# Optimization experiments

Hardware: AMD Instinct MI355X
Metric: run time of the kernel (lower is better)

The kernel has to match this reference:

```python
import jax, jax.numpy as jnp
import numpy as np

N, E, D, H, C = 100000, 1600000, 128, 256, 40


def setup_inputs() -> dict:
    key = jax.random.key(0)
    ks = jax.random.split(key, 10)
    x = jax.random.normal(ks[0], (N, D), dtype=jnp.float32)
    src = jax.random.randint(ks[1], (E,), 0, N, dtype=jnp.int32)
    dst = jax.random.randint(ks[2], (E,), 0, N, dtype=jnp.int32)
    # GIN layer 1 MLP (bias-free), kaiming-uniform-like scale 1/sqrt(fan_in)
    w1a = jax.random.normal(ks[3], (D, H), dtype=jnp.float32) / np.sqrt(D)
    w1b = jax.random.normal(ks[4], (H, H), dtype=jnp.float32) / np.sqrt(H)
    # GIN layer 2 MLP
    w2a = jax.random.normal(ks[5], (H, H), dtype=jnp.float32) / np.sqrt(H)
    w2b = jax.random.normal(ks[6], (H, H), dtype=jnp.float32) / np.sqrt(H)
    # eps initialized to 0 per reset_parameters
    eps1 = jnp.zeros((), dtype=jnp.float32)
    eps2 = jnp.zeros((), dtype=jnp.float32)
    # final classifier fc (with bias)
    fc_w = jax.random.normal(ks[7], (H, C), dtype=jnp.float32) / np.sqrt(H)
    fc_b = jax.random.normal(ks[8], (C,), dtype=jnp.float32) * 0.01
    return {"x": x, "src": src, "dst": dst,
            "eps1": eps1, "w1a": w1a, "w1b": w1b,
            "eps2": eps2, "w2a": w2a, "w2b": w2b,
            "fc_w": fc_w, "fc_b": fc_b}


def reference(x, src, dst, eps1, w1a, w1b, eps2, w2a, w2b, fc_w, fc_b):
    n = x.shape[0]

    def gin_layer(h, eps, wa, wb):
        # GINConv sum-aggregation: scatter-add neighbor feats over edges
        agg = jax.ops.segment_sum(h[src], dst, num_segments=n)  # [N, d]
        rst = (1.0 + eps) * h + agg
        # 2-layer bias-free MLP with ReLU between
        return jax.nn.relu(rst @ wa) @ wb

    h = jax.nn.relu(gin_layer(x, eps1, w1a, w1b))   # layer + outer activation
    h = jax.nn.relu(gin_layer(h, eps2, w2a, w2b))   # dropout p=0 -> identity
    return h @ fc_w + fc_b                           # [N, C]
```

## Files before the change

### kernel.cpp

```cpp
#include <hip/hip_runtime.h>

#define N_NODES 100000
#define N_EDGES 1600000
#define DIM_IN  128
#define DIM_H   256
#define DIM_C   40

#define NB   391
#define NBLK 391
#define CHUNK 4096
#define ECAP 6144

#define CVT_BLOCKS 25000
#define WCVT_BLOCKS 1280

typedef unsigned short bf16_t;
typedef __attribute__((ext_vector_type(8))) short short8;
typedef __attribute__((ext_vector_type(4))) float f32x4;

__device__ __forceinline__ bf16_t f2b(float f) {
    unsigned int u = __float_as_uint(f);
    unsigned int r = (u + 0x7fffu + ((u >> 16) & 1u)) >> 16;
    return (bf16_t)r;
}

__device__ __forceinline__ void gl_lds16(const void* gsrc, void* ldst) {
    __builtin_amdgcn_global_load_lds(
        (const __attribute__((address_space(1))) void*)gsrc,
        (__attribute__((address_space(3))) void*)ldst,
        16, 0, 0);
}


__global__ __launch_bounds__(256) void k_prep(
    const int* __restrict__ dst, int* __restrict__ cnt2,
    const float* __restrict__ x, signed char* __restrict__ x8, float* __restrict__ xs,
    const float* __restrict__ w1a, const float* __restrict__ w1b,
    const float* __restrict__ w2a, const float* __restrict__ w2b,
    const float* __restrict__ fcw,
    bf16_t* __restrict__ o1a, bf16_t* __restrict__ o1b,
    bf16_t* __restrict__ o2a, bf16_t* __restrict__ o2b, bf16_t* __restrict__ ofc,
    int* __restrict__ ticket)
{
    __shared__ int h[NB];
    int blk = blockIdx.x, t = threadIdx.x;

    if (blk < NBLK) {
        if (blk == 0 && t == 0) *ticket = 0;
        for (int i = t; i < NB; i += 256) h[i] = 0;
        __syncthreads();
        int base = blk * CHUNK;
        int end = min(base + CHUNK, N_EDGES);
        for (int i = base + t; i < end; i += 256)
            atomicAdd(&h[dst[i] >> 8], 1);
        __syncthreads();
        for (int i = t; i < NB; i += 256) cnt2[blk * NB + i] = h[i];
        return;
    }
    blk -= NBLK;

    if (blk < CVT_BLOCKS) {
        int gid = blk * 256 + t;
        int u = gid >> 6, lane = gid & 63;
        float2 v = *(const float2*)(x + (size_t)u * 128 + lane * 2);
        float m = fmaxf(fabsf(v.x), fabsf(v.y));
        #pragma unroll
        for (int d = 1; d < 64; d <<= 1)
            m = fmaxf(m, __shfl_xor(m, d, 64));
        float inv = (m > 0.f) ? 127.f / m : 0.f;
        int q0 = (int)rintf(v.x * inv);
        int q1 = (int)rintf(v.y * inv);
        unsigned short pk = (unsigned short)((q0 & 0xff) | ((q1 & 0xff) << 8));
        *(unsigned short*)(x8 + ((unsigned)u << 7) + lane * 2) = pk;
        if (lane == 0) xs[u] = (m > 0.f) ? m * (1.f / 127.f) : 0.f;
        return;
    }
    blk -= CVT_BLOCKS;

    int r = blk >> 8;
    int idx = (blk & 255) * 256 + t;
    const float* in; bf16_t* out; int K, N, Npad;
    switch (r) {
        case 0: in = w1a; out = o1a; K = 128; N = 256; Npad = 256; break;
        case 1: in = w1b; out = o1b; K = 256; N = 256; Npad = 256; break;
        case 2: in = w2a; out = o2a; K = 256; N = 256; Npad = 256; break;
        case 3: in = w2b; out = o2b; K = 256; N = 256; Npad = 256; break;
        default: in = fcw; out = ofc; K = 256; N = 40;  Npad = 128; break;
    }
    if (idx >= Npad * K) return;
    int n = idx / K, k = idx - n * K;
    float v = (n < N) ? in[(size_t)k * N + n] : 0.f;
    out[idx] = f2b(v);
}


__global__ void k_bscanA(const int* __restrict__ cnt2, int* __restrict__ basep,
                         int* __restrict__ btot, int* __restrict__ ticket,
                         int* __restrict__ boff) {
    __shared__ int s[512];
    __shared__ int isLast;
    int t = threadIdx.x, b = blockIdx.x;
    int v = (t < NBLK) ? cnt2[t * NB + b] : 0;
    s[t] = v;
    __syncthreads();
    #pragma unroll
    for (int d = 1; d < 512; d <<= 1) {
        int tv = (t >= d) ? s[t - d] : 0;
        __syncthreads();
        s[t] += tv;
        __syncthreads();
    }
    if (t < NBLK) basep[t * NB + b] = s[t] - v;
    if (t == 511) atomicExch(&btot[b], s[511]);
    __syncthreads();
    if (t == 0) {
        __threadfence();
        int old = atomicAdd(ticket, 1);
        isLast = (old == NB - 1);
    }
    __syncthreads();
    if (!isLast) return;

    __threadfence();
    int v2 = (t < NB) ? atomicAdd(&btot[t], 0) : 0;
    s[t] = v2;
    __syncthreads();
    #pragma unroll
    for (int d = 1; d < 512; d <<= 1) {
        int tv = (t >= d) ? s[t - d] : 0;
        __syncthreads();
        s[t] += tv;
        __syncthreads();
    }
    if (t < NB) boff[t] = s[t] - v2;
    if (t == NB - 1) boff[NB] = s[t];
}

__global__ void k_bscatter(const int* __restrict__ src, const int* __restrict__ dst,
                           const int* __restrict__ basep, const int* __restrict__ boff,
                           int* __restrict__ ebuf, int e) {
    __shared__ int cur[NB];
    int t = threadIdx.x, blk = blockIdx.x;
    for (int i = t; i < NB; i += 256) cur[i] = basep[blk * NB + i] + boff[i];
    __syncthreads();
    int base = blk * CHUNK;
    int end = min(base + CHUNK, e);
    for (int i = base + t; i < end; i += 256) {
        int sv = src[i], dv = dst[i];
        int pos = atomicAdd(&cur[dv >> 8], 1);
        ebuf[pos] = sv | ((dv & 255) << 24);
    }
}

__global__ __launch_bounds__(256) void k_build(const int* __restrict__ ebuf,
                                               const int* __restrict__ boff,
                                               int* __restrict__ off,
                                               int* __restrict__ csr) {
    __shared__ int ec[ECAP];
    __shared__ int h[256];
    __shared__ int cur[256];
    int t = threadIdx.x, b = blockIdx.x;
    int node0 = b << 8;
    int e0 = boff[b], e1 = boff[b + 1];
    int ne = e1 - e0;
    bool fits = (ne <= ECAP);
    h[t] = 0;
    __syncthreads();
    if (fits) {
        for (int i = t; i < ne; i += 256) {
            int p = ebuf[e0 + i];
            ec[i] = p;
            atomicAdd(&h[(unsigned)p >> 24], 1);
        }
    } else {
        for (int i = t; i < ne; i += 256)
            atomicAdd(&h[(unsigned)ebuf[e0 + i] >> 24], 1);
    }
    __syncthreads();
    int mydeg = h[t];
    #pragma unroll
    for (int d = 1; d < 256; d <<= 1) {
        int tv = (t >= d) ? h[t - d] : 0;
        __syncthreads();
        h[t] += tv;
        __syncthreads();
    }
    int node = node0 + t;
    if (node < N_NODES) off[node + 1] = e0 + h[t];
    if (b == 0 && t == 0) off[0] = 0;
    cur[t] = e0 + h[t] - mydeg;
    __syncthreads();
    if (fits) {
        for (int i = t; i < ne; i += 256) {
            int p = ec[i];
            int pos = atomicAdd(&cur[(unsigned)p >> 24], 1);
            csr[pos] = p & 0xFFFFFF;
        }
    } else {
        for (int i = t; i < ne; i += 256) {
            int p = ebuf[e0 + i];
            int pos = atomicAdd(&cur[(unsigned)p >> 24], 1);
            csr[pos] = p & 0xFFFFFF;
        }
    }
}


__global__ void k_agg_i8(const signed char* __restrict__ h8, const float* __restrict__ hs,
                         const int* __restrict__ off, const int* __restrict__ csr,
                         const float* __restrict__ eps_p,
                         bf16_t* __restrict__ rst, int n) {
    int gid = blockIdx.x * blockDim.x + threadIdx.x;
    int u = __builtin_amdgcn_readfirstlane(gid >> 6);
    int lane = threadIdx.x & 63;
    if (u >= n) return;

    float acc0 = 0.f, acc1 = 0.f;
    int r0 = off[u], r1 = off[u + 1];
    unsigned loff = lane * 2u;

    for (int base = r0; base < r1; base += 64) {
        int m = r1 - base; if (m > 64) m = 64;
        int li = (lane < m) ? lane : (m - 1);
        int iv = csr[base + li];
        for (int c = 0; c < m; c += 16) {
            int s[16]; float sc[16]; unsigned v[16];
            #pragma unroll
            for (int t = 0; t < 16; t++)
                s[t] = __builtin_amdgcn_readlane(iv, c + t);
            #pragma unroll
            for (int t = 0; t < 16; t++)
                sc[t] = (c + t < m) ? hs[s[t]] : 0.f;
            #pragma unroll
            for (int t = 0; t < 16; t++)
                v[t] = *(const unsigned short*)(h8 + (((unsigned)s[t] << 7) + loff));
            #pragma unroll
            for (int t = 0; t < 16; t++) {
                acc0 += (float)(int)(signed char)(v[t] & 0xffu) * sc[t];
                acc1 += (float)(int)(signed char)(v[t] >> 8) * sc[t];
            }
        }
    }

    float scu = hs[u] * (1.0f + eps_p[0]);
    unsigned vu = *(const unsigned short*)(h8 + (((unsigned)u << 7) + loff));
    float o0 = (float)(int)(signed char)(vu & 0xffu) * scu + acc0;
    float o1 = (float)(int)(signed char)(vu >> 8) * scu + acc1;
    *(unsigned int*)(rst + ((unsigned)u << 7) + lane * 2) =
        (unsigned int)f2b(o0) | ((unsigned int)f2b(o1) << 16);
}


__global__ void k_agg_u8(const unsigned char* __restrict__ h8,
                         const float* __restrict__ hs,
                         const int* __restrict__ off, const int* __restrict__ csr,
                         const float* __restrict__ eps_p,
                         bf16_t* __restrict__ rst, int n) {
    int gid = blockIdx.x * blockDim.x + threadIdx.x;
    int u = __builtin_amdgcn_readfirstlane(gid >> 6);
    int lane = threadIdx.x & 63;
    if (u >= n) return;

    float acc[4] = {0.f, 0.f, 0.f, 0.f};
    int r0 = off[u], r1 = off[u + 1];
    unsigned loff = lane * 4u;

    for (int base = r0; base < r1; base += 64) {
        int m = r1 - base; if (m > 64) m = 64;
        int li = (lane < m) ? lane : (m - 1);
        int iv = csr[base + li];
        for (int c = 0; c < m; c += 16) {
            int s[16]; float sc[16]; unsigned int v[16];
            #pragma unroll
            for (int t = 0; t < 16; t++)
                s[t] = __builtin_amdgcn_readlane(iv, c + t);
            #pragma unroll
            for (int t = 0; t < 16; t++)
                sc[t] = (c + t < m) ? hs[s[t]] : 0.f;
            #pragma unroll
            for (int t = 0; t < 16; t++)
                v[t] = *(const unsigned int*)(h8 + (((unsigned)s[t] << 8) + loff));
            #pragma unroll
            for (int t = 0; t < 16; t++) {
                acc[0] += (float)(v[t] & 0xffu) * sc[t];
                acc[1] += (float)((v[t] >> 8) & 0xffu) * sc[t];
                acc[2] += (float)((v[t] >> 16) & 0xffu) * sc[t];
                acc[3] += (float)(v[t] >> 24) * sc[t];
            }
        }
    }

    float ep = 1.0f + eps_p[0];
    unsigned int vu = *(const unsigned int*)(h8 + (((unsigned)u << 8) + loff));
    float scu = hs[u] * ep;
    float o0 = (float)(vu & 0xffu) * scu + acc[0];
    float o1 = (float)((vu >> 8) & 0xffu) * scu + acc[1];
    float o2 = (float)((vu >> 16) & 0xffu) * scu + acc[2];
    float o3 = (float)(vu >> 24) * scu + acc[3];
    uint2 ov;
    ov.x = (unsigned int)f2b(o0) | ((unsigned int)f2b(o1) << 16);
    ov.y = (unsigned int)f2b(o2) | ((unsigned int)f2b(o3) << 16);
    *(uint2*)(rst + (size_t)u * 256 + lane * 4) = ov;
}


#define TS_STRIDE 264

template <int K1, bool OUT8, bool FUSE_FC>
__global__ __launch_bounds__(512, 4) void k_mlp(
    const bf16_t* __restrict__ A, const bf16_t* __restrict__ W1t,
    const bf16_t* __restrict__ W2t, bf16_t* __restrict__ H,
    unsigned char* __restrict__ H8, float* __restrict__ Hs,
    const bf16_t* __restrict__ FCt, const float* __restrict__ fc_b,
    float* __restrict__ Cout, int M)
{
    __shared__ __align__(16) bf16_t As[2][64 * 32];
    __shared__ __align__(16) bf16_t Bs[2][256 * 32];
    __shared__ __align__(16) bf16_t Ts[64 * TS_STRIDE];
    __shared__ int rmax[64];

    int tid = threadIdx.x;
    int wave = tid >> 6, lane = tid & 63;
    int l15 = lane & 15, quad = lane >> 4;
    int bm = blockIdx.x * 64;
    int wn = wave * 32;

    auto stage1 = [&](int k0, int b) {
        if (tid < 256) {
            int row = tid >> 2, k8 = (tid & 3) * 8;
            int gr = bm + row; if (gr >= M) gr = M - 1;
            gl_lds16(A + (size_t)gr * K1 + k0 + k8, &As[b][tid * 8]);
        }
        {
            int c = tid;
            int row = c >> 2, k8 = (c & 3) * 8;
            gl_lds16(W1t + (size_t)row * K1 + k0 + k8, &Bs[b][c * 8]);
        }
        {
            int c = tid + 512;
            int row = c >> 2, k8 = (c & 3) * 8;
            gl_lds16(W1t + (size_t)row * K1 + k0 + k8, &Bs[b][c * 8]);
        }
    };
    auto stage2 = [&](int k0, int b) {
        {
            int c = tid;
            int row = c >> 2, k8 = (c & 3) * 8;
            gl_lds16(W2t + (size_t)row * 256 + k0 + k8, &Bs[b][c * 8]);
        }
        {
            int c = tid + 512;
            int row = c >> 2, k8 = (c & 3) * 8;
            gl_lds16(W2t + (size_t)row * 256 + k0 + k8, &Bs[b][c * 8]);
        }
    };

    f32x4 acc[4][2];
    #pragma unroll
    for (int i = 0; i < 4; i++)
        #pragma unroll
        for (int j = 0; j < 2; j++) acc[i][j] = 0.f;

    constexpr int NS1 = K1 / 32;
    stage1(0, 0);
    for (int k = 0; k < NS1; k++) {
        int cur = k & 1;
        if (k + 1 < NS1) {
            stage1((k + 1) * 32, cur ^ 1);
            if (tid < 256) { asm volatile("s_waitcnt vmcnt(3)" ::: "memory"); }
            else           { asm volatile("s_waitcnt vmcnt(2)" ::: "memory"); }
        } else {
            asm volatile("s_waitcnt vmcnt(0)" ::: "memory");
        }
        __builtin_amdgcn_sched_barrier(0);
        __builtin_amdgcn_s_barrier();

        short8 af[4], bfv[2];
        #pragma unroll
        for (int i = 0; i < 4; i++)
            af[i] = *(const short8*)&As[cur][(i * 16 + l15) * 32 + quad * 8];
        #pragma unroll
        for (int j = 0; j < 2; j++)
            bfv[j] = *(const short8*)&Bs[cur][(wn + j * 16 + l15) * 32 + quad * 8];

        #pragma unroll
        for (int i = 0; i < 4; i++)
            #pragma unroll
            for (int j = 0; j < 2; j++)
                acc[i][j] = __builtin_amdgcn_mfma_f32_16x16x32_bf16(af[i], bfv[j], acc[i][j], 0, 0, 0);

        asm volatile("s_waitcnt lgkmcnt(0)" ::: "memory");
        __builtin_amdgcn_sched_barrier(0);
        __builtin_amdgcn_s_barrier();
    }

    #pragma unroll
    for (int i = 0; i < 4; i++)
        #pragma unroll
        for (int j = 0; j < 2; j++) {
            int row = i * 16 + quad * 4;
            int col = wn + j * 16 + l15;
            #pragma unroll
            for (int r = 0; r < 4; r++)
                Ts[(row + r) * TS_STRIDE + col] = f2b(fmaxf(acc[i][j][r], 0.f));
        }

    #pragma unroll
    for (int i = 0; i < 4; i++)
        #pragma unroll
        for (int j = 0; j < 2; j++) acc[i][j] = 0.f;
    __syncthreads();

    stage2(0, 0);
    for (int k = 0; k < 8; k++) {
        int cur = k & 1;
        if (k + 1 < 8) {
            stage2((k + 1) * 32, cur ^ 1);
            asm volatile("s_waitcnt vmcnt(2)" ::: "memory");
        } else {
            asm volatile("s_waitcnt vmcnt(0)" ::: "memory");
        }
        __builtin_amdgcn_sched_barrier(0);
        __builtin_amdgcn_s_barrier();

        short8 af[4], bfv[2];
        #pragma unroll
        for (int i = 0; i < 4; i++)
            af[i] = *(const short8*)&Ts[(i * 16 + l15) * TS_STRIDE + k * 32 + quad * 8];
        #pragma unroll
        for (int j = 0; j < 2; j++)
            bfv[j] = *(const short8*)&Bs[cur][(wn + j * 16 + l15) * 32 + quad * 8];

        #pragma unroll
        for (int i = 0; i < 4; i++)
            #pragma unroll
            for (int j = 0; j < 2; j++)
                acc[i][j] = __builtin_amdgcn_mfma_f32_16x16x32_bf16(af[i], bfv[j], acc[i][j], 0, 0, 0);

        asm volatile("s_waitcnt lgkmcnt(0)" ::: "memory");
        __builtin_amdgcn_sched_barrier(0);
        __builtin_amdgcn_s_barrier();
    }

    if constexpr (OUT8) {
        if (tid < 64) rmax[tid] = 0;
        __syncthreads();
        #pragma unroll
        for (int i = 0; i < 4; i++)
            #pragma unroll
            for (int r = 0; r < 4; r++) {
                float m = 0.f;
                #pragma unroll
                for (int j = 0; j < 2; j++) m = fmaxf(m, acc[i][j][r]);
                atomicMax(&rmax[i * 16 + quad * 4 + r], __float_as_int(m));
            }
        __syncthreads();
        #pragma unroll
        for (int i = 0; i < 4; i++) {
            #pragma unroll
            for (int r = 0; r < 4; r++) {
                int row = i * 16 + quad * 4 + r;
                int rowg = bm + row;
                if (rowg >= M) continue;
                float rm = __int_as_float(rmax[row]);
                float inv = (rm > 0.f) ? 255.f / rm : 0.f;
                #pragma unroll
                for (int j = 0; j < 2; j++) {
                    int col = wn + j * 16 + l15;
                    float v = fmaxf(acc[i][j][r], 0.f);
                    unsigned q = (unsigned)(v * inv + 0.5f);
                    if (q > 255u) q = 255u;
                    H8[(size_t)rowg * 256 + col] = (unsigned char)q;
                }
                if (wave == 0 && l15 == 0)
                    Hs[rowg] = rm * (1.f / 255.f);
            }
        }
    } else if constexpr (FUSE_FC) {
        #pragma unroll
        for (int i = 0; i < 4; i++)
            #pragma unroll
            for (int j = 0; j < 2; j++) {
                int row = i * 16 + quad * 4;
                int col = wn + j * 16 + l15;
                #pragma unroll
                for (int r = 0; r < 4; r++)
                    Ts[(row + r) * TS_STRIDE + col] = f2b(fmaxf(acc[i][j][r], 0.f));
            }
        __syncthreads();

        f32x4 acc3[3];
        #pragma unroll
        for (int j = 0; j < 3; j++) acc3[j] = 0.f;

        auto stage3 = [&](int k0, int b) {
            if (tid < 256) {
                int row = tid >> 2, k8 = (tid & 3) * 8;
                gl_lds16(FCt + (size_t)row * 256 + k0 + k8, &Bs[b][tid * 8]);
            }
        };

        stage3(0, 0);
        for (int k = 0; k < 8; k++) {
            int cur = k & 1;
            if (k + 1 < 8) {
                stage3((k + 1) * 32, cur ^ 1);
                if (tid < 256) { asm volatile("s_waitcnt vmcnt(1)" ::: "memory"); }
            } else {
                if (tid < 256) { asm volatile("s_waitcnt vmcnt(0)" ::: "memory"); }
            }
            __builtin_amdgcn_sched_barrier(0);
            __builtin_amdgcn_s_barrier();

            if (tid < 256) {
                short8 af = *(const short8*)&Ts[(wave * 16 + l15) * TS_STRIDE + k * 32 + quad * 8];
                #pragma unroll
                for (int j = 0; j < 3; j++) {
                    short8 bfv = *(const short8*)&Bs[cur][(j * 16 + l15) * 32 + quad * 8];
                    acc3[j] = __builtin_amdgcn_mfma_f32_16x16x32_bf16(af, bfv, acc3[j], 0, 0, 0);
                }
                asm volatile("s_waitcnt lgkmcnt(0)" ::: "memory");
            }
            __builtin_amdgcn_sched_barrier(0);
            __builtin_amdgcn_s_barrier();
        }

        if (tid < 256) {
            #pragma unroll
            for (int j = 0; j < 3; j++) {
                int col = j * 16 + l15;
                if (col >= DIM_C) continue;
                float bv = fc_b[col];
                #pragma unroll
                for (int r = 0; r < 4; r++) {
                    int rowg = bm + wave * 16 + quad * 4 + r;
                    if (rowg < M)
                        Cout[(size_t)rowg * DIM_C + col] = acc3[j][r] + bv;
                }
            }
        }
    } else {
        #pragma unroll
        for (int j = 0; j < 2; j++) {
            int col = wn + j * 16 + l15;
            #pragma unroll
            for (int i = 0; i < 4; i++) {
                #pragma unroll
                for (int r = 0; r < 4; r++) {
                    int rowg = bm + i * 16 + quad * 4 + r;
                    if (rowg < M)
                        H[(size_t)rowg * 256 + col] = f2b(fmaxf(acc[i][j][r], 0.f));
                }
            }
        }
    }
}


static inline size_t rnd256(size_t x) { return (x + 255) & ~(size_t)255; }

extern "C" void kernel_launch(void* const* d_in, const int* in_sizes, int n_in,
                              void* d_out, int out_size, void* d_ws, size_t ws_size,
                              hipStream_t stream) {
    const float* x    = (const float*)d_in[0];
    const int*   src  = (const int*)d_in[1];
    const int*   dst  = (const int*)d_in[2];
    const float* eps1 = (const float*)d_in[3];
    const float* w1a  = (const float*)d_in[4];
    const float* w1b  = (const float*)d_in[5];
    const float* eps2 = (const float*)d_in[6];
    const float* w2a  = (const float*)d_in[7];
    const float* w2b  = (const float*)d_in[8];
    const float* fc_w = (const float*)d_in[9];
    const float* fc_b = (const float*)d_in[10];
    float* out = (float*)d_out;

    char* w = (char*)d_ws;
    int* off  = (int*)w; w += rnd256(sizeof(int) * (size_t)(N_NODES + 1));
    int* csr  = (int*)w; w += rnd256(sizeof(int) * (size_t)N_EDGES);
    int* cnt2  = (int*)w; w += rnd256(sizeof(int) * (size_t)NBLK * NB);
    int* basep = (int*)w; w += rnd256(sizeof(int) * (size_t)NBLK * NB);
    int* btot  = (int*)w; w += rnd256(sizeof(int) * 512);
    int* boff  = (int*)w; w += rnd256(sizeof(int) * (NB + 1));
    bf16_t* w1a_t = (bf16_t*)w; w += rnd256(2 * (size_t)DIM_H * DIM_IN);
    bf16_t* w1b_t = (bf16_t*)w; w += rnd256(2 * (size_t)DIM_H * DIM_H);
    bf16_t* w2a_t = (bf16_t*)w; w += rnd256(2 * (size_t)DIM_H * DIM_H);
    bf16_t* w2b_t = (bf16_t*)w; w += rnd256(2 * (size_t)DIM_H * DIM_H);
    bf16_t* fc_t  = (bf16_t*)w; w += rnd256(2 * (size_t)128 * DIM_H);
    signed char* x8 = (signed char*)w; w += rnd256((size_t)N_NODES * DIM_IN);
    float* xs = (float*)w; w += rnd256(sizeof(float) * (size_t)N_NODES);
    unsigned char* h8 = (unsigned char*)w; w += rnd256((size_t)N_NODES * DIM_H);
    float* hs = (float*)w; w += rnd256(sizeof(float) * (size_t)N_NODES);
    bf16_t* R12 = (bf16_t*)w; w += rnd256(2 * (size_t)N_NODES * DIM_H);
    bf16_t* R3  = (bf16_t*)w; w += rnd256(2 * (size_t)N_NODES * DIM_H);

    bf16_t* rst1 = R12;
    int* ebuf = (int*)R3;
    int* ticket = btot + 500;

    k_prep<<<NBLK + CVT_BLOCKS + WCVT_BLOCKS, 256, 0, stream>>>(
        dst, cnt2, x, x8, xs, w1a, w1b, w2a, w2b, fc_w,
        w1a_t, w1b_t, w2a_t, w2b_t, fc_t, ticket);

    k_bscanA<<<NB, 512, 0, stream>>>(cnt2, basep, btot, ticket, boff);
    k_bscatter<<<NBLK, 256, 0, stream>>>(src, dst, basep, boff, ebuf, N_EDGES);
    k_build<<<NB, 256, 0, stream>>>(ebuf, boff, off, csr);

    const int agg_blocks = (N_NODES * 64 + 255) / 256;
    const int mlp_blocks = (N_NODES + 63) / 64;

    k_agg_i8<<<agg_blocks, 256, 0, stream>>>(x8, xs, off, csr, eps1, rst1, N_NODES);
    k_mlp<DIM_IN, true, false><<<mlp_blocks, 512, 0, stream>>>(
        rst1, w1a_t, w1b_t, nullptr, h8, hs, nullptr, nullptr, nullptr, N_NODES);

    k_agg_u8<<<agg_blocks, 256, 0, stream>>>(h8, hs, off, csr, eps2, (bf16_t*)R3, N_NODES);
    k_mlp<DIM_H, false, true><<<mlp_blocks, 512, 0, stream>>>(
        (bf16_t*)R3, w2a_t, w2b_t, nullptr, nullptr, nullptr, fc_t, fc_b, out, N_NODES);
}
```

Before: 421.4 us.

## Pre-swizzle weights into MFMA fragment layout and load A directly into registers

```diff
diff --git a/kernel.cpp b/kernel.cpp
--- a/kernel.cpp
+++ b/kernel.cpp
@@ -85,12 +85,15 @@
         case 1: in = w1b; out = o1b; K = 256; N = 256; Npad = 256; break;
         case 2: in = w2a; out = o2a; K = 256; N = 256; Npad = 256; break;
         case 3: in = w2b; out = o2b; K = 256; N = 256; Npad = 256; break;
-        default: in = fcw; out = ofc; K = 256; N = 40;  Npad = 128; break;
+        default: in = fcw; out = ofc; K = 256; N = 40;  Npad = 64;  break;
     }
     if (idx >= Npad * K) return;
     int n = idx / K, k = idx - n * K;
     float v = (n < N) ? in[(size_t)k * N + n] : 0.f;
-    out[idx] = f2b(v);
+    int kstep = k >> 5, quad = (k >> 3) & 3, e = k & 7;
+    int tt = n >> 4, l15 = n & 15;
+    size_t opos = (size_t)kstep * (Npad * 32) + ((tt * 4 + quad) * 16 + l15) * 8 + e;
+    out[opos] = f2b(v);
 }
 
 
@@ -307,14 +310,13 @@
 #define TS_STRIDE 264
 
 template <int K1, bool OUT8, bool FUSE_FC>
-__global__ __launch_bounds__(512, 4) void k_mlp(
+__global__ __launch_bounds__(256, 2) void k_mlp(
     const bf16_t* __restrict__ A, const bf16_t* __restrict__ W1t,
     const bf16_t* __restrict__ W2t, bf16_t* __restrict__ H,
     unsigned char* __restrict__ H8, float* __restrict__ Hs,
     const bf16_t* __restrict__ FCt, const float* __restrict__ fc_b,
     float* __restrict__ Cout, int M)
 {
-    __shared__ __align__(16) bf16_t As[2][64 * 32];
     __shared__ __align__(16) bf16_t Bs[2][256 * 32];
     __shared__ __align__(16) bf16_t Ts[64 * TS_STRIDE];
     __shared__ int rmax[64];
@@ -323,81 +325,65 @@
     int wave = tid >> 6, lane = tid & 63;
     int l15 = lane & 15, quad = lane >> 4;
     int bm = blockIdx.x * 64;
-    int wn = wave * 32;
-
-    auto stage1 = [&](int k0, int b) {
-        if (tid < 256) {
-            int row = tid >> 2, k8 = (tid & 3) * 8;
-            int gr = bm + row; if (gr >= M) gr = M - 1;
-            gl_lds16(A + (size_t)gr * K1 + k0 + k8, &As[b][tid * 8]);
-        }
-        {
-            int c = tid;
-            int row = c >> 2, k8 = (c & 3) * 8;
-            gl_lds16(W1t + (size_t)row * K1 + k0 + k8, &Bs[b][c * 8]);
-        }
-        {
-            int c = tid + 512;
-            int row = c >> 2, k8 = (c & 3) * 8;
-            gl_lds16(W1t + (size_t)row * K1 + k0 + k8, &Bs[b][c * 8]);
+
+    auto stageB = [&](const bf16_t* W, int kstep, int b) {
+        #pragma unroll
+        for (int l = 0; l < 4; l++) {
+            int c = l * 256 + tid;
+            gl_lds16(W + ((size_t)kstep * 1024 + c) * 8, &Bs[b][c * 8]);
         }
     };
-    auto stage2 = [&](int k0, int b) {
-        {
-            int c = tid;
-            int row = c >> 2, k8 = (c & 3) * 8;
-            gl_lds16(W2t + (size_t)row * 256 + k0 + k8, &Bs[b][c * 8]);
-        }
-        {
-            int c = tid + 512;
-            int row = c >> 2, k8 = (c & 3) * 8;
-            gl_lds16(W2t + (size_t)row * 256 + k0 + k8, &Bs[b][c * 8]);
-        }
-    };
-
-    f32x4 acc[4][2];
+
+    f32x4 acc[4][4];
     #pragma unroll
     for (int i = 0; i < 4; i++)
         #pragma unroll
-        for (int j = 0; j < 2; j++) acc[i][j] = 0.f;
+        for (int j = 0; j < 4; j++) acc[i][j] = 0.f;
 
     constexpr int NS1 = K1 / 32;
-    stage1(0, 0);
+    short8 afr[NS1][4];
+    #pragma unroll
+    for (int ks = 0; ks < NS1; ks++)
+        #pragma unroll
+        for (int i = 0; i < 4; i++) {
+            int gr = bm + i * 16 + l15; if (gr >= M) gr = M - 1;
+            afr[ks][i] = *(const short8*)(A + (size_t)gr * K1 + ks * 32 + quad * 8);
+        }
+
+    stageB(W1t, 0, 0);
+    #pragma unroll
     for (int k = 0; k < NS1; k++) {
         int cur = k & 1;
         if (k + 1 < NS1) {
-            stage1((k + 1) * 32, cur ^ 1);
-            if (tid < 256) { asm volatile("s_waitcnt vmcnt(3)" ::: "memory"); }
-            else           { asm volatile("s_waitcnt vmcnt(2)" ::: "memory"); }
+            stageB(W1t, k + 1, cur ^ 1);
+            asm volatile("s_waitcnt vmcnt(4)" ::: "memory");
         } else {
             asm volatile("s_waitcnt vmcnt(0)" ::: "memory");
         }
         __builtin_amdgcn_sched_barrier(0);
         __builtin_amdgcn_s_barrier();
 
-        short8 af[4], bfv[2];
+        short8 bfv[4];
+        #pragma unroll
+        for (int j = 0; j < 4; j++)
+            bfv[j] = *(const short8*)&Bs[cur][((wave * 4 + j) * 64 + lane) * 8];
+
         #pragma unroll
         for (int i = 0; i < 4; i++)
-            af[i] = *(const short8*)&As[cur][(i * 16 + l15) * 32 + quad * 8];
-        #pragma unroll
-        for (int j = 0; j < 2; j++)
-            bfv[j] = *(const short8*)&Bs[cur][(wn + j * 16 + l15) * 32 + quad * 8];
-
-        #pragma unroll
-        for (int i = 0; i < 4; i++)
-            #pragma unroll
-            for (int j = 0; j < 2; j++)
-                acc[i][j] = __builtin_amdgcn_mfma_f32_16x16x32_bf16(af[i], bfv[j], acc[i][j], 0, 0, 0);
+            #pragma unroll
+            for (int j = 0; j < 4; j++)
+                acc[i][j] = __builtin_amdgcn_mfma_f32_16x16x32_bf16(afr[k][i], bfv[j], acc[i][j], 0, 0, 0);
 
         asm volatile("s_waitcnt lgkmcnt(0)" ::: "memory");
         __builtin_amdgcn_sched_barrier(0);
         __builtin_amdgcn_s_barrier();
     }
 
+    int wn = wave * 64;
     #pragma unroll
     for (int i = 0; i < 4; i++)
         #pragma unroll
-        for (int j = 0; j < 2; j++) {
+        for (int j = 0; j < 4; j++) {
             int row = i * 16 + quad * 4;
             int col = wn + j * 16 + l15;
             #pragma unroll
@@ -408,33 +394,34 @@
     #pragma unroll
     for (int i = 0; i < 4; i++)
         #pragma unroll
-        for (int j = 0; j < 2; j++) acc[i][j] = 0.f;
-    __syncthreads();
-
-    stage2(0, 0);
+        for (int j = 0; j < 4; j++) acc[i][j] = 0.f;
+    __syncthreads();
+
+    stageB(W2t, 0, 0);
+    #pragma unroll
     for (int k = 0; k < 8; k++) {
         int cur = k & 1;
         if (k + 1 < 8) {
-            stage2((k + 1) * 32, cur ^ 1);
-            asm volatile("s_waitcnt vmcnt(2)" ::: "memory");
+            stageB(W2t, k + 1, cur ^ 1);
+            asm volatile("s_waitcnt vmcnt(4)" ::: "memory");
         } else {
             asm volatile("s_waitcnt vmcnt(0)" ::: "memory");
         }
         __builtin_amdgcn_sched_barrier(0);
         __builtin_amdgcn_s_barrier();
 
-        short8 af[4], bfv[2];
+        short8 af[4], bfv[4];
         #pragma unroll
         for (int i = 0; i < 4; i++)
             af[i] = *(const short8*)&Ts[(i * 16 + l15) * TS_STRIDE + k * 32 + quad * 8];
         #pragma unroll
-        for (int j = 0; j < 2; j++)
-            bfv[j] = *(const short8*)&Bs[cur][(wn + j * 16 + l15) * 32 + quad * 8];
+        for (int j = 0; j < 4; j++)
+            bfv[j] = *(const short8*)&Bs[cur][((wave * 4 + j) * 64 + lane) * 8];
 
         #pragma unroll
         for (int i = 0; i < 4; i++)
             #pragma unroll
-            for (int j = 0; j < 2; j++)
+            for (int j = 0; j < 4; j++)
                 acc[i][j] = __builtin_amdgcn_mfma_f32_16x16x32_bf16(af[i], bfv[j], acc[i][j], 0, 0, 0);
 
         asm volatile("s_waitcnt lgkmcnt(0)" ::: "memory");
@@ -451,7 +438,7 @@
             for (int r = 0; r < 4; r++) {
                 float m = 0.f;
                 #pragma unroll
-                for (int j = 0; j < 2; j++) m = fmaxf(m, acc[i][j][r]);
+                for (int j = 0; j < 4; j++) m = fmaxf(m, acc[i][j][r]);
                 atomicMax(&rmax[i * 16 + quad * 4 + r], __float_as_int(m));
             }
         __syncthreads();
@@ -465,7 +452,7 @@
                 float rm = __int_as_float(rmax[row]);
                 float inv = (rm > 0.f) ? 255.f / rm : 0.f;
                 #pragma unroll
-                for (int j = 0; j < 2; j++) {
+                for (int j = 0; j < 4; j++) {
                     int col = wn + j * 16 + l15;
                     float v = fmaxf(acc[i][j][r], 0.f);
                     unsigned q = (unsigned)(v * inv + 0.5f);
@@ -480,7 +467,7 @@
         #pragma unroll
         for (int i = 0; i < 4; i++)
             #pragma unroll
-            for (int j = 0; j < 2; j++) {
+            for (int j = 0; j < 4; j++) {
                 int row = i * 16 + quad * 4;
                 int col = wn + j * 16 + l15;
                 #pragma unroll
@@ -493,55 +480,50 @@
         #pragma unroll
         for (int j = 0; j < 3; j++) acc3[j] = 0.f;
 
-        auto stage3 = [&](int k0, int b) {
-            if (tid < 256) {
-                int row = tid >> 2, k8 = (tid & 3) * 8;
-                gl_lds16(FCt + (size_t)row * 256 + k0 + k8, &Bs[b][tid * 8]);
-            }
+        auto stage3 = [&](int kstep, int b) {
+            gl_lds16(FCt + ((size_t)kstep * 256 + tid) * 8, &Bs[b][tid * 8]);
         };
 
         stage3(0, 0);
+        #pragma unroll
         for (int k = 0; k < 8; k++) {
             int cur = k & 1;
             if (k + 1 < 8) {
-                stage3((k + 1) * 32, cur ^ 1);
-                if (tid < 256) { asm volatile("s_waitcnt vmcnt(1)" ::: "memory"); }
+                stage3(k + 1, cur ^ 1);
+                asm volatile("s_waitcnt vmcnt(1)" ::: "memory");
             } else {
-                if (tid < 256) { asm volatile("s_waitcnt vmcnt(0)" ::: "memory"); }
+                asm volatile("s_waitcnt vmcnt(0)" ::: "memory");
             }
             __builtin_amdgcn_sched_barrier(0);
             __builtin_amdgcn_s_barrier();
 
-            if (tid < 256) {
-                short8 af = *(const short8*)&Ts[(wave * 16 + l15) * TS_STRIDE + k * 32 + quad * 8];
-                #pragma unroll
-                for (int j = 0; j < 3; j++) {
-                    short8 bfv = *(const short8*)&Bs[cur][(j * 16 + l15) * 32 + quad * 8];
-                    acc3[j] = __builtin_amdgcn_mfma_f32_16x16x32_bf16(af, bfv, acc3[j], 0, 0, 0);
-                }
-                asm volatile("s_waitcnt lgkmcnt(0)" ::: "memory");
-            }
+            short8 af = *(const short8*)&Ts[(wave * 16 + l15) * TS_STRIDE + k * 32 + quad * 8];
+            #pragma unroll
+            for (int j = 0; j < 3; j++) {
+                short8 bfv = *(const short8*)&Bs[cur][((j * 64) + lane) * 8];
+                acc3[j] = __builtin_amdgcn_mfma_f32_16x16x32_bf16(af, bfv, acc3[j], 0, 0, 0);
+            }
+
+            asm volatile("s_waitcnt lgkmcnt(0)" ::: "memory");
             __builtin_amdgcn_sched_barrier(0);
             __builtin_amdgcn_s_barrier();
         }
 
-        if (tid < 256) {
-            #pragma unroll
-            for (int j = 0; j < 3; j++) {
-                int col = j * 16 + l15;
-                if (col >= DIM_C) continue;
-                float bv = fc_b[col];
-                #pragma unroll
-                for (int r = 0; r < 4; r++) {
-                    int rowg = bm + wave * 16 + quad * 4 + r;
-                    if (rowg < M)
-                        Cout[(size_t)rowg * DIM_C + col] = acc3[j][r] + bv;
-                }
+        #pragma unroll
+        for (int j = 0; j < 3; j++) {
+            int col = j * 16 + l15;
+            if (col >= DIM_C) continue;
+            float bv = fc_b[col];
+            #pragma unroll
+            for (int r = 0; r < 4; r++) {
+                int rowg = bm + wave * 16 + quad * 4 + r;
+                if (rowg < M)
+                    Cout[(size_t)rowg * DIM_C + col] = acc3[j][r] + bv;
             }
         }
     } else {
         #pragma unroll
-        for (int j = 0; j < 2; j++) {
+        for (int j = 0; j < 4; j++) {
             int col = wn + j * 16 + l15;
             #pragma unroll
             for (int i = 0; i < 4; i++) {
@@ -610,10 +592,10 @@
     const int mlp_blocks = (N_NODES + 63) / 64;
 
     k_agg_i8<<<agg_blocks, 256, 0, stream>>>(x8, xs, off, csr, eps1, rst1, N_NODES);
-    k_mlp<DIM_IN, true, false><<<mlp_blocks, 512, 0, stream>>>(
+    k_mlp<DIM_IN, true, false><<<mlp_blocks, 256, 0, stream>>>(
         rst1, w1a_t, w1b_t, nullptr, h8, hs, nullptr, nullptr, nullptr, N_NODES);
 
     k_agg_u8<<<agg_blocks, 256, 0, stream>>>(h8, hs, off, csr, eps2, (bf16_t*)R3, N_NODES);
-    k_mlp<DIM_H, false, true><<<mlp_blocks, 512, 0, stream>>>(
+    k_mlp<DIM_H, false, true><<<mlp_blocks, 256, 0, stream>>>(
         (bf16_t*)R3, w2a_t, w2b_t, nullptr, nullptr, nullptr, fc_t, fc_b, out, N_NODES);
 }
```

Result: no change. 429.1 us (+1.8%).
